# Kernel optimization log

Hardware: AMD Instinct MI355X
Metric: run time of the kernel (lower is better)

Reference implementation:

```python
import jax, jax.numpy as jnp
import numpy as np

TEMPERATURE = 0.2
HYPER_GAMMA = 0.5
EPS = 1e-12  # torch F.normalize / cosine_similarity eps guard (1e-12 / 1e-8)

def setup_inputs() -> dict:
    key = jax.random.key(0)
    k1, k2 = jax.random.split(key)
    B, D = 4096, 1024
    return {
        "emb_i": jax.random.normal(k1, (B, D), dtype=jnp.float32),
        "emb_j": jax.random.normal(k2, (B, D), dtype=jnp.float32),
    }

def _l2_normalize(x, eps=EPS):
    n = jnp.sqrt(jnp.sum(x * x, axis=1, keepdims=True))
    return x / jnp.maximum(n, eps)

def reference(emb_i, emb_j):
    B = emb_i.shape[0]
    z_i = _l2_normalize(emb_i)
    z_j = _l2_normalize(emb_j)
    # cosine similarity of unit vectors == dot product; sim[a, b] = <z_j[a], z_i[b]>
    sim = jnp.einsum('ad,bd->ab', z_j, z_i)  # [B, B]
    sim_positive = jnp.diagonal(sim)
    positives_exp = jnp.exp(-sim_positive + TEMPERATURE)
    neg_mask = 1.0 - jnp.eye(B, dtype=sim.dtype)
    negatives_exp = neg_mask * jnp.exp(sim - TEMPERATURE)
    positives_sum = jnp.sum(jnp.log1p(positives_exp)) / B
    negatives_sum = jnp.sum(jnp.log1p(negatives_exp)) / (B * (B - 1))
    return HYPER_GAMMA * positives_sum + (1.0 - HYPER_GAMMA) * negatives_sum
```

## Files before the change

kernel.cpp:

```cpp
#include <hip/hip_runtime.h>
#include <math.h>

#define B_ROWS 4096
#define D_DIM  1024
static constexpr float TEMP = 0.2f;

typedef __attribute__((ext_vector_type(8))) short bf16x8;
typedef __attribute__((ext_vector_type(4))) float f32x4;

__device__ inline unsigned short f2bf(float f) {
    unsigned int u = __float_as_uint(f);
    u += 0x7fffu + ((u >> 16) & 1u);
    return (unsigned short)(u >> 16);
}

__device__ inline void gload_lds16(const unsigned short* g, unsigned short* l) {
    __builtin_amdgcn_global_load_lds(
        (const __attribute__((address_space(1))) unsigned int*)g,
        (__attribute__((address_space(3))) unsigned int*)l,
        16, 0, 0);
}


__global__ __launch_bounds__(256) void norm_cast_kernel(
        const float* __restrict__ emb_i, const float* __restrict__ emb_j,
        unsigned short* __restrict__ Zi, unsigned short* __restrict__ Zj,
        float* __restrict__ w) {
    const int tid = threadIdx.x;
    if (blockIdx.x == 0 && tid == 0) {
        w[0] = 0.0f; w[1] = 0.0f;
        ((unsigned int*)w)[2] = 0u;
    }
    const int wave = tid >> 6, lane = tid & 63;
    const int row = blockIdx.x * 4 + wave;
    const float* src; unsigned short* dst; int r;
    if (row < B_ROWS) { src = emb_i; dst = Zi; r = row; }
    else              { src = emb_j; dst = Zj; r = row - B_ROWS; }

    const float4* p = (const float4*)(src + (size_t)r * D_DIM);
    float4 v0 = p[lane], v1 = p[64 + lane], v2 = p[128 + lane], v3 = p[192 + lane];
    float s = v0.x*v0.x + v0.y*v0.y + v0.z*v0.z + v0.w*v0.w
            + v1.x*v1.x + v1.y*v1.y + v1.z*v1.z + v1.w*v1.w
            + v2.x*v2.x + v2.y*v2.y + v2.z*v2.z + v2.w*v2.w
            + v3.x*v3.x + v3.y*v3.y + v3.z*v3.z + v3.w*v3.w;
    #pragma unroll
    for (int m = 1; m < 64; m <<= 1) s += __shfl_xor(s, m, 64);
    const float inv = 1.0f / fmaxf(sqrtf(s), 1e-12f);

    ushort4* q = (ushort4*)(dst + (size_t)r * D_DIM);
    ushort4 o0 = { f2bf(v0.x*inv), f2bf(v0.y*inv), f2bf(v0.z*inv), f2bf(v0.w*inv) };
    ushort4 o1 = { f2bf(v1.x*inv), f2bf(v1.y*inv), f2bf(v1.z*inv), f2bf(v1.w*inv) };
    ushort4 o2 = { f2bf(v2.x*inv), f2bf(v2.y*inv), f2bf(v2.z*inv), f2bf(v2.w*inv) };
    ushort4 o3 = { f2bf(v3.x*inv), f2bf(v3.y*inv), f2bf(v3.z*inv), f2bf(v3.w*inv) };
    q[lane] = o0; q[64 + lane] = o1; q[128 + lane] = o2; q[192 + lane] = o3;
}

__global__ __launch_bounds__(256, 4) void simloss_mfma_kernel(
        const unsigned short* __restrict__ Zi,
        const unsigned short* __restrict__ Zj,
        float* __restrict__ w, float* __restrict__ out) {
    __shared__ __align__(16) unsigned short lA[128 * 64];
    __shared__ __align__(16) unsigned short lB[128 * 64];
    __shared__ float rn[4], rp[4];

    const int tid  = threadIdx.x;
    const int lane = tid & 63;
    const int wave = tid >> 6;
    const int wy = wave >> 1, wx = wave & 1;
    const int rowBase = blockIdx.y * 128;
    const int colBase = blockIdx.x * 128;

    const int lrow = lane >> 3;
    const int lp   = lane & 7;
    const int lc   = (lp - lrow) & 7;
    const unsigned short* gA = Zj + (size_t)(rowBase + wave * 32 + lrow) * D_DIM + lc * 8;
    const unsigned short* gB = Zi + (size_t)(colBase + wave * 32 + lrow) * D_DIM + lc * 8;
    unsigned short* sA = lA + wave * 4 * 512;
    unsigned short* sB = lB + wave * 4 * 512;

    const int fr = lane & 15;
    const int p0 = ((lane >> 4) + (lane & 7)) & 7;
    const int p1 = (p0 + 4) & 7;
    const unsigned short* fA0 = lA + (wy * 64 + fr) * 64 + p0 * 8;
    const unsigned short* fA1 = lA + (wy * 64 + fr) * 64 + p1 * 8;
    const unsigned short* fB0 = lB + (wx * 64 + fr) * 64 + p0 * 8;
    const unsigned short* fB1 = lB + (wx * 64 + fr) * 64 + p1 * 8;

    f32x4 acc[4][4];
    #pragma unroll
    for (int i = 0; i < 4; ++i)
        #pragma unroll
        for (int j = 0; j < 4; ++j)
            acc[i][j] = (f32x4){0.f, 0.f, 0.f, 0.f};

    for (int k0 = 0; k0 < D_DIM; k0 += 64) {
        __syncthreads();
        #pragma unroll
        for (int ch = 0; ch < 4; ++ch) {
            gload_lds16(gA + ch * 8 * D_DIM, sA + ch * 512);
            gload_lds16(gB + ch * 8 * D_DIM, sB + ch * 512);
        }
        gA += 64; gB += 64;
        __syncthreads();

        bf16x8 a[4], b[4];
        #pragma unroll
        for (int i = 0; i < 4; ++i) a[i] = *(const bf16x8*)(fA0 + i * 1024);
        #pragma unroll
        for (int j = 0; j < 4; ++j) b[j] = *(const bf16x8*)(fB0 + j * 1024);
        #pragma unroll
        for (int i = 0; i < 4; ++i)
            #pragma unroll
            for (int j = 0; j < 4; ++j)
                acc[i][j] = __builtin_amdgcn_mfma_f32_16x16x32_bf16(
                    a[i], b[j], acc[i][j], 0, 0, 0);
        #pragma unroll
        for (int i = 0; i < 4; ++i) a[i] = *(const bf16x8*)(fA1 + i * 1024);
        #pragma unroll
        for (int j = 0; j < 4; ++j) b[j] = *(const bf16x8*)(fB1 + j * 1024);
        #pragma unroll
        for (int i = 0; i < 4; ++i)
            #pragma unroll
            for (int j = 0; j < 4; ++j)
                acc[i][j] = __builtin_amdgcn_mfma_f32_16x16x32_bf16(
                    a[i], b[j], acc[i][j], 0, 0, 0);
    }

    const int cr = (lane >> 4) * 4;
    const int cc = lane & 15;
    float neg = 0.f, pos = 0.f;
    #pragma unroll
    for (int i = 0; i < 4; ++i) {
        const int abase = rowBase + wy * 64 + i * 16 + cr;
        #pragma unroll
        for (int j = 0; j < 4; ++j) {
            const int b = colBase + wx * 64 + j * 16 + cc;
            #pragma unroll
            for (int r = 0; r < 4; ++r) {
                const float x = acc[i][j][r] - TEMP;
                if (abase + r == b) pos += __logf(1.0f + __expf(-x));
                else                neg += __logf(1.0f + __expf(x));
            }
        }
    }
    #pragma unroll
    for (int off = 32; off > 0; off >>= 1) {
        neg += __shfl_down(neg, off, 64);
        pos += __shfl_down(pos, off, 64);
    }
    if (lane == 0) { rn[wave] = neg; rp[wave] = pos; }
    __syncthreads();
    if (tid == 0) {
        atomicAdd(&w[1], rn[0] + rn[1] + rn[2] + rn[3]);
        if (blockIdx.x == blockIdx.y)
            atomicAdd(&w[0], rp[0] + rp[1] + rp[2] + rp[3]);
        __threadfence();
        unsigned int done = atomicAdd(((unsigned int*)w) + 2, 1u);
        if (done == gridDim.x * gridDim.y - 1) {
            const float psum = atomicAdd(&w[0], 0.0f);
            const float nsum = atomicAdd(&w[1], 0.0f);
            out[0] = 0.5f * (psum / (float)B_ROWS)
                   + 0.5f * (nsum / ((float)B_ROWS * (float)(B_ROWS - 1)));
        }
    }
}

extern "C" void kernel_launch(void* const* d_in, const int* in_sizes, int n_in,
                              void* d_out, int out_size, void* d_ws, size_t ws_size,
                              hipStream_t stream) {
    const float* emb_i = (const float*)d_in[0];
    const float* emb_j = (const float*)d_in[1];
    float* w = (float*)d_ws;
    unsigned short* Zi = (unsigned short*)(w + 16);
    unsigned short* Zj = Zi + (size_t)B_ROWS * D_DIM;
    float* out = (float*)d_out;

    norm_cast_kernel<<<2 * B_ROWS / 4, 256, 0, stream>>>(emb_i, emb_j, Zi, Zj, w);
    dim3 grid(B_ROWS / 128, B_ROWS / 128);
    simloss_mfma_kernel<<<grid, 256, 0, stream>>>(Zi, Zj, w, out);
}
```

Baseline: 147.0 us.

## Widen GEMM tile to 128x256 with K-step 32 and fewer blocks

The similarity GEMM tile grows from 128x128 to 128x256, so each wave accumulates a 64x128 sub-tile (4x8 MFMA fragments). The K step per LDS stage drops from 64 to 32, and the swizzle and load mapping are changed to match. Occupancy bounds are relaxed from 4 to 2 blocks per SM. This raises arithmetic intensity per LDS load and halves the grid, in exchange for more registers, lower occupancy, and twice as many sync barriers per K.

```diff
diff --git a/kernel.cpp b/kernel.cpp
--- a/kernel.cpp
+++ b/kernel.cpp
@@ -55,12 +55,12 @@
     q[lane] = o0; q[64 + lane] = o1; q[128 + lane] = o2; q[192 + lane] = o3;
 }
 
-__global__ __launch_bounds__(256, 4) void simloss_mfma_kernel(
+__global__ __launch_bounds__(256, 2) void simloss_mfma_kernel(
         const unsigned short* __restrict__ Zi,
         const unsigned short* __restrict__ Zj,
         float* __restrict__ w, float* __restrict__ out) {
-    __shared__ __align__(16) unsigned short lA[128 * 64];
-    __shared__ __align__(16) unsigned short lB[128 * 64];
+    __shared__ __align__(16) unsigned short lA[128 * 32];
+    __shared__ __align__(16) unsigned short lB[256 * 32];
     __shared__ float rn[4], rp[4];
 
     const int tid  = threadIdx.x;
@@ -68,73 +68,67 @@
     const int wave = tid >> 6;
     const int wy = wave >> 1, wx = wave & 1;
     const int rowBase = blockIdx.y * 128;
-    const int colBase = blockIdx.x * 128;
+    const int colBase = blockIdx.x * 256;
 
-    const int lrow = lane >> 3;
-    const int lp   = lane & 7;
-    const int lc   = (lp - lrow) & 7;
-    const unsigned short* gA = Zj + (size_t)(rowBase + wave * 32 + lrow) * D_DIM + lc * 8;
-    const unsigned short* gB = Zi + (size_t)(colBase + wave * 32 + lrow) * D_DIM + lc * 8;
-    unsigned short* sA = lA + wave * 4 * 512;
-    unsigned short* sB = lB + wave * 4 * 512;
+    const int lrow = lane >> 2;
+    const int lp   = lane & 3;
+    const int lc   = (lp - (lrow >> 1)) & 3;
+    const unsigned short* gA0 = Zj + (size_t)(rowBase + (2*wave+0)*16 + lrow) * D_DIM + lc*8;
+    const unsigned short* gA1 = Zj + (size_t)(rowBase + (2*wave+1)*16 + lrow) * D_DIM + lc*8;
+    const unsigned short* gB0 = Zi + (size_t)(colBase + (4*wave+0)*16 + lrow) * D_DIM + lc*8;
+    const unsigned short* gB1 = Zi + (size_t)(colBase + (4*wave+1)*16 + lrow) * D_DIM + lc*8;
+    const unsigned short* gB2 = Zi + (size_t)(colBase + (4*wave+2)*16 + lrow) * D_DIM + lc*8;
+    const unsigned short* gB3 = Zi + (size_t)(colBase + (4*wave+3)*16 + lrow) * D_DIM + lc*8;
+    unsigned short* sA0 = lA + (2*wave+0) * 512;
+    unsigned short* sA1 = lA + (2*wave+1) * 512;
+    unsigned short* sB0 = lB + (4*wave+0) * 512;
+    unsigned short* sB1 = lB + (4*wave+1) * 512;
+    unsigned short* sB2 = lB + (4*wave+2) * 512;
+    unsigned short* sB3 = lB + (4*wave+3) * 512;
 
     const int fr = lane & 15;
-    const int p0 = ((lane >> 4) + (lane & 7)) & 7;
-    const int p1 = (p0 + 4) & 7;
-    const unsigned short* fA0 = lA + (wy * 64 + fr) * 64 + p0 * 8;
-    const unsigned short* fA1 = lA + (wy * 64 + fr) * 64 + p1 * 8;
-    const unsigned short* fB0 = lB + (wx * 64 + fr) * 64 + p0 * 8;
-    const unsigned short* fB1 = lB + (wx * 64 + fr) * 64 + p1 * 8;
+    const int q4 = lane >> 4;
+    const int p0 = (q4 + (fr >> 1)) & 3;
+    const unsigned short* fA = lA + (wy * 64 + fr) * 32 + p0 * 8;
+    const unsigned short* fB = lB + (wx * 128 + fr) * 32 + p0 * 8;
 
-    f32x4 acc[4][4];
+    f32x4 acc[4][8];
     #pragma unroll
     for (int i = 0; i < 4; ++i)
         #pragma unroll
-        for (int j = 0; j < 4; ++j)
+        for (int j = 0; j < 8; ++j)
             acc[i][j] = (f32x4){0.f, 0.f, 0.f, 0.f};
 
-    for (int k0 = 0; k0 < D_DIM; k0 += 64) {
+    for (int k0 = 0; k0 < D_DIM; k0 += 32) {
         __syncthreads();
-        #pragma unroll
-        for (int ch = 0; ch < 4; ++ch) {
-            gload_lds16(gA + ch * 8 * D_DIM, sA + ch * 512);
-            gload_lds16(gB + ch * 8 * D_DIM, sB + ch * 512);
-        }
-        gA += 64; gB += 64;
+        gload_lds16(gA0, sA0); gload_lds16(gA1, sA1);
+        gload_lds16(gB0, sB0); gload_lds16(gB1, sB1);
+        gload_lds16(gB2, sB2); gload_lds16(gB3, sB3);
+        gA0 += 32; gA1 += 32; gB0 += 32; gB1 += 32; gB2 += 32; gB3 += 32;
         __syncthreads();
 
-        bf16x8 a[4], b[4];
+        bf16x8 a[4], b[8];
         #pragma unroll
-        for (int i = 0; i < 4; ++i) a[i] = *(const bf16x8*)(fA0 + i * 1024);
+        for (int i = 0; i < 4; ++i) a[i] = *(const bf16x8*)(fA + i * 16 * 32);
         #pragma unroll
-        for (int j = 0; j < 4; ++j) b[j] = *(const bf16x8*)(fB0 + j * 1024);
+        for (int j = 0; j < 8; ++j) b[j] = *(const bf16x8*)(fB + j * 16 * 32);
         #pragma unroll
         for (int i = 0; i < 4; ++i)
             #pragma unroll
-            for (int j = 0; j < 4; ++j)
-                acc[i][j] = __builtin_amdgcn_mfma_f32_16x16x32_bf16(
-                    a[i], b[j], acc[i][j], 0, 0, 0);
-        #pragma unroll
-        for (int i = 0; i < 4; ++i) a[i] = *(const bf16x8*)(fA1 + i * 1024);
-        #pragma unroll
-        for (int j = 0; j < 4; ++j) b[j] = *(const bf16x8*)(fB1 + j * 1024);
-        #pragma unroll
-        for (int i = 0; i < 4; ++i)
-            #pragma unroll
-            for (int j = 0; j < 4; ++j)
+            for (int j = 0; j < 8; ++j)
                 acc[i][j] = __builtin_amdgcn_mfma_f32_16x16x32_bf16(
                     a[i], b[j], acc[i][j], 0, 0, 0);
     }
 
-    const int cr = (lane >> 4) * 4;
+    const int cr = q4 * 4;
     const int cc = lane & 15;
     float neg = 0.f, pos = 0.f;
     #pragma unroll
     for (int i = 0; i < 4; ++i) {
         const int abase = rowBase + wy * 64 + i * 16 + cr;
         #pragma unroll
-        for (int j = 0; j < 4; ++j) {
-            const int b = colBase + wx * 64 + j * 16 + cc;
+        for (int j = 0; j < 8; ++j) {
+            const int b = colBase + wx * 128 + j * 16 + cc;
             #pragma unroll
             for (int r = 0; r < 4; ++r) {
                 const float x = acc[i][j][r] - TEMP;
@@ -152,7 +146,7 @@
     __syncthreads();
     if (tid == 0) {
         atomicAdd(&w[1], rn[0] + rn[1] + rn[2] + rn[3]);
-        if (blockIdx.x == blockIdx.y)
+        if ((int)blockIdx.x == (int)(blockIdx.y >> 1))
             atomicAdd(&w[0], rp[0] + rp[1] + rp[2] + rp[3]);
         __threadfence();
         unsigned int done = atomicAdd(((unsigned int*)w) + 2, 1u);
@@ -176,6 +170,6 @@
     float* out = (float*)d_out;
 
     norm_cast_kernel<<<2 * B_ROWS / 4, 256, 0, stream>>>(emb_i, emb_j, Zi, Zj, w);
-    dim3 grid(B_ROWS / 128, B_ROWS / 128);
+    dim3 grid(B_ROWS / 256, B_ROWS / 128);
     simloss_mfma_kernel<<<grid, 256, 0, stream>>>(Zi, Zj, w, out);
 }
```

Measured after the change: 125.9 us. -14.4%, faster.
